# Optimization experiments

Hardware: AMD Instinct MI355X
Metric: run time of the kernel (lower is better)

## Reference

```python
import jax, jax.numpy as jnp
import numpy as np

K = 4          # neighbor_num
BN_EPS = 1e-5


def setup_inputs() -> dict:
    key = jax.random.key(0)
    ks = jax.random.split(key, 5)
    b, n, c = 16384, 12, 512
    x = jax.random.normal(ks[0], (b, n, c), dtype=jnp.float32)
    std = np.sqrt(2.0 / c).astype(np.float32)
    Uw = jax.random.normal(ks[1], (c, c), dtype=jnp.float32) * std
    Vw = jax.random.normal(ks[2], (c, c), dtype=jnp.float32) * std
    bound = 1.0 / np.sqrt(c)
    Ub = jax.random.uniform(ks[3], (c,), minval=-bound, maxval=bound, dtype=jnp.float32)
    Vb = jax.random.uniform(ks[4], (c,), minval=-bound, maxval=bound, dtype=jnp.float32)
    gamma = jnp.ones((n,), dtype=jnp.float32)
    beta = jnp.zeros((n,), dtype=jnp.float32)
    return {"x": x, "Uw": Uw, "Ub": Ub, "Vw": Vw, "Vb": Vb, "gamma": gamma, "beta": beta}


def reference(x, Uw, Ub, Vw, Vb, gamma, beta):
    # x: [b, n, c] with n = num_classes nodes
    # ---- dynamic top-k adjacency ('dots' metric), built on detached x ----
    si = jax.lax.stop_gradient(x)
    sim = jnp.einsum('bic,bjc->bij', si, si)                 # [b, n, n]
    thr = jax.lax.top_k(sim, K)[0][..., -1:]                 # k-th largest per row
    adj = (sim >= thr).astype(x.dtype)                       # [b, n, n]
    # ---- normalize_digraph: D^{-1/2} A D^{-1/2} (row degrees) ----
    deg_inv_sqrt = adj.sum(axis=-1) ** -0.5                  # [b, n]
    A = deg_inv_sqrt[:, :, None] * adj * deg_inv_sqrt[:, None, :]
    # ---- aggregate + projections ----
    Vx = jnp.einsum('bnc,dc->bnd', x, Vw) + Vb               # V(x)
    agg = jnp.einsum('bij,bjc->bic', A, Vx)
    h = agg + jnp.einsum('bnc,dc->bnd', x, Uw) + Ub          # aggregate + U(x)
    # ---- BatchNorm1d over node channel n (stats over batch and feature dims) ----
    mean = h.mean(axis=(0, 2))                               # [n]
    var = ((h - mean[None, :, None]) ** 2).mean(axis=(0, 2)) # biased var, [n]
    hn = (h - mean[None, :, None]) * jax.lax.rsqrt(var + BN_EPS)[None, :, None]
    hn = hn * gamma[None, :, None] + beta[None, :, None]
    return jax.nn.relu(x + hn)
```

## Files before the change

### kernel.cpp

```cpp
#include <hip/hip_runtime.h>
#include <hip/hip_fp16.h>


typedef _Float16 half8 __attribute__((ext_vector_type(8)));
typedef _Float16 half4 __attribute__((ext_vector_type(4)));
typedef float floatx4 __attribute__((ext_vector_type(4)));

#define NN 12
#define CH 512
#define NB 16384
#define M_ROWS (NB * NN)

__device__ __forceinline__ float relu_f(float v) { return v > 0.f ? v : 0.f; }

__device__ __forceinline__ void gload16(const void* g, void* l) {
    __builtin_amdgcn_global_load_lds(
        (__attribute__((address_space(1))) const unsigned int*)g,
        (__attribute__((address_space(3))) unsigned int*)l, 16, 0, 0);
}

__global__ __launch_bounds__(256) void kw_build(const float* __restrict__ Uw,
                                                const float* __restrict__ Vw,
                                                _Float16* __restrict__ Wcat,
                                                double* __restrict__ gAcc) {
    int e = blockIdx.x * 256 + threadIdx.x;
    int d = e >> 10, k = e & 1023;
    float v = (k < 512) ? Uw[d * 512 + k] : Vw[d * 512 + (k - 512)];
    Wcat[e] = (_Float16)v;
    if (blockIdx.x == 0 && threadIdx.x < 24) gAcc[threadIdx.x] = 0.0;
}

__global__ __launch_bounds__(256) void k1_adj(const float* __restrict__ x,
                                              _Float16* __restrict__ Abuf,
                                              float* __restrict__ rs,
                                              int pathA) {
    __shared__ float xs[NN][CH + 4];
    __shared__ double sim[NN][NN];
    __shared__ double thr[NN];
    __shared__ float Amat[NN][NN];
    __shared__ float dinv[NN];

    const int b = blockIdx.x, t = threadIdx.x;
    const float* xb = x + (size_t)b * NN * CH;

    for (int e = t; e < NN * CH / 4; e += 256) {
        int r = e >> 7, c4 = (e & 127) << 2;
        float4 v = ((const float4*)xb)[e];
        *(float4*)&xs[r][c4] = v;
    }
    __syncthreads();

    if (t < 78) {
        int i = 0, rem = t;
        while (rem >= NN - i) { rem -= NN - i; i++; }
        const int j = i + rem;
        double a0 = 0.0, a1 = 0.0, a2 = 0.0, a3 = 0.0;
        for (int c = 0; c < CH; c += 4) {
            float4 va = *(const float4*)&xs[i][c];
            float4 vb = *(const float4*)&xs[j][c];
            a0 += (double)va.x * (double)vb.x;
            a1 += (double)va.y * (double)vb.y;
            a2 += (double)va.z * (double)vb.z;
            a3 += (double)va.w * (double)vb.w;
        }
        double acc = (a0 + a1) + (a2 + a3);
        sim[i][j] = acc;
        sim[j][i] = acc;
    }
    __syncthreads();

    if (t < 12) {
        double a = -1e300, b2 = -1e300, c2 = -1e300, d2 = -1e300;
        for (int j = 0; j < 12; j++) {
            double v = sim[t][j];
            if (v > a)       { d2 = c2; c2 = b2; b2 = a; a = v; }
            else if (v > b2) { d2 = c2; c2 = b2; b2 = v; }
            else if (v > c2) { d2 = c2; c2 = v; }
            else if (v > d2) { d2 = v; }
        }
        thr[t] = d2;
        int deg = 0;
        for (int j = 0; j < 12; j++) deg += (sim[t][j] >= d2);
        dinv[t] = 1.0f / sqrtf((float)deg);
    }
    __syncthreads();

    if (t < 144) {
        int i = t / 12, j = t % 12;
        Amat[i][j] = (sim[i][j] >= thr[i]) ? dinv[i] * dinv[j] : 0.0f;
    }
    __syncthreads();

    if (t < 12) {
        float s = 0.f;
        for (int j = 0; j < 12; j++) s += Amat[t][j];
        rs[b * NN + t] = s;
    }

    const size_t strideK = pathA ? 1024 : 512;
    const size_t yoff = pathA ? 512 : 0;
    for (int e = t; e < NN * CH / 4; e += 256) {
        int i = e >> 7, c4 = (e & 127) << 2;
        float ax = 0.f, ay = 0.f, az = 0.f, aw = 0.f;
#pragma unroll
        for (int j = 0; j < 12; j++) {
            const float a = Amat[i][j];
            float4 v = *(const float4*)&xs[j][c4];
            ax += a * v.x; ay += a * v.y; az += a * v.z; aw += a * v.w;
        }
        const size_t row = (size_t)b * NN + i;
        half4 hy;
        hy[0] = (_Float16)ax; hy[1] = (_Float16)ay;
        hy[2] = (_Float16)az; hy[3] = (_Float16)aw;
        *(half4*)(Abuf + row * strideK + yoff + c4) = hy;
        if (pathA) {
            float4 xv = *(const float4*)&xs[i][c4];
            half4 hx;
            hx[0] = (_Float16)xv.x; hx[1] = (_Float16)xv.y;
            hx[2] = (_Float16)xv.z; hx[3] = (_Float16)xv.w;
            *(half4*)(Abuf + row * 1024 + c4) = hx;
        }
    }
}

__global__ __launch_bounds__(256) void k2_gemm(
    const _Float16* __restrict__ Abuf, const float* __restrict__ xf,
    const _Float16* __restrict__ Wcat, const float* __restrict__ rs,
    const float* __restrict__ Ub, const float* __restrict__ Vb,
    float* __restrict__ hout, double* __restrict__ gS1,
    double* __restrict__ gS2, int pathA) {
    __shared__ __align__(16) _Float16 As[128 * 32];
    __shared__ __align__(16) _Float16 Bs[128 * 32];
    __shared__ float bs1[12], bs2[12];

    const int t = threadIdx.x;
    const int bid = blockIdx.x;
    const int xcd = bid & 7, jj = bid >> 3;
    const int nt = jj & 3, mt = (jj >> 2) * 8 + xcd;
    const int m0 = mt * 128, n0 = nt * 128;
    const int lane = t & 63, wv = t >> 6;
    const int l15 = lane & 15, quad = lane >> 4;
    const int mwb = (wv & 1) * 64, nwb = (wv >> 1) * 64;
    const int srow = t >> 2, scol = (t & 3) * 8;

    _Float16* ldsA = As + wv * 512;
    _Float16* ldsB = Bs + wv * 512;

    floatx4 acc[4][4];
#pragma unroll
    for (int mi = 0; mi < 4; mi++)
#pragma unroll
        for (int ni = 0; ni < 4; ni++)
#pragma unroll
            for (int e = 0; e < 4; e++) acc[mi][ni][e] = 0.f;

    for (int kt = 0; kt < 32; kt++) {
        const int k0 = kt * 32;
        __syncthreads();
        if (pathA) {
#pragma unroll
            for (int pass = 0; pass < 2; pass++) {
                const int row = srow + pass * 64;
                const size_t grow = (size_t)(m0 + row);
                gload16(Abuf + grow * 1024 + k0 + scol, ldsA + pass * 2048);
                gload16(Wcat + (size_t)(n0 + row) * 1024 + k0 + scol,
                        ldsB + pass * 2048);
            }
        } else {
#pragma unroll
            for (int pass = 0; pass < 2; pass++) {
                const int row = srow + pass * 64;
                const size_t grow = (size_t)(m0 + row);
                if (k0 < 512) {
                    const float* p = xf + grow * 512 + k0 + scol;
                    float4 f0 = *(const float4*)p;
                    float4 f1 = *(const float4*)(p + 4);
                    half8 va;
                    va[0] = (_Float16)f0.x; va[1] = (_Float16)f0.y;
                    va[2] = (_Float16)f0.z; va[3] = (_Float16)f0.w;
                    va[4] = (_Float16)f1.x; va[5] = (_Float16)f1.y;
                    va[6] = (_Float16)f1.z; va[7] = (_Float16)f1.w;
                    *(half8*)&As[row * 32 + scol] = va;
                } else {
                    gload16(Abuf + grow * 512 + (k0 - 512) + scol,
                            ldsA + pass * 2048);
                }
                gload16(Wcat + (size_t)(n0 + row) * 1024 + k0 + scol,
                        ldsB + pass * 2048);
            }
        }
        __syncthreads();

        half8 af[4], bfr[4];
#pragma unroll
        for (int mi = 0; mi < 4; mi++)
            af[mi] = *(half8*)&As[(mwb + mi * 16 + l15) * 32 + quad * 8];
#pragma unroll
        for (int ni = 0; ni < 4; ni++)
            bfr[ni] = *(half8*)&Bs[(nwb + ni * 16 + l15) * 32 + quad * 8];
#pragma unroll
        for (int mi = 0; mi < 4; mi++)
#pragma unroll
            for (int ni = 0; ni < 4; ni++)
                acc[mi][ni] = __builtin_amdgcn_mfma_f32_16x16x32_f16(
                    af[mi], bfr[ni], acc[mi][ni], 0, 0, 0);
    }

    if (t < 12) { bs1[t] = 0.f; bs2[t] = 0.f; }
    __syncthreads();
#pragma unroll
    for (int mi = 0; mi < 4; mi++) {
#pragma unroll
        for (int r = 0; r < 4; r++) {
            const int m = m0 + mwb + mi * 16 + quad * 4 + r;
            const float rsm = rs[m];
            float p1 = 0.f, p2 = 0.f;
#pragma unroll
            for (int ni = 0; ni < 4; ni++) {
                const int d = n0 + nwb + ni * 16 + l15;
                float h = acc[mi][ni][r] + rsm * Vb[d] + Ub[d];
                hout[(size_t)m * 512 + d] = h;
                p1 += h; p2 += h * h;
            }
            for (int off = 1; off < 16; off <<= 1) {
                p1 += __shfl_xor(p1, off, 16);
                p2 += __shfl_xor(p2, off, 16);
            }
            if (l15 == 0) {
                atomicAdd(&bs1[m % 12], p1);
                atomicAdd(&bs2[m % 12], p2);
            }
        }
    }
    __syncthreads();
    if (t < 12) {
        atomicAdd(&gS1[t], (double)bs1[t]);
        atomicAdd(&gS2[t], (double)bs2[t]);
    }
}

__global__ void k3_stats(const double* __restrict__ gS1,
                         const double* __restrict__ gS2,
                         const float* __restrict__ gamma,
                         const float* __restrict__ beta,
                         float* __restrict__ bnp) {
    int t = threadIdx.x;
    if (t < 12) {
        const double cnt = (double)NB * 512.0;
        double mean = gS1[t] / cnt;
        double var = gS2[t] / cnt - mean * mean;
        float inv = rsqrtf((float)var + 1e-5f);
        float scale = gamma[t] * inv;
        bnp[t] = scale;
        bnp[12 + t] = beta[t] - (float)mean * scale;
    }
}

__global__ __launch_bounds__(256) void k4_final(const float* __restrict__ x,
                                                float* __restrict__ out,
                                                const float* __restrict__ bnp) {
    __shared__ float sc[12], sh[12];
    if (threadIdx.x < 12) {
        sc[threadIdx.x] = bnp[threadIdx.x];
        sh[threadIdx.x] = bnp[12 + threadIdx.x];
    }
    __syncthreads();
    const size_t n4 = (size_t)M_ROWS * 128;
    for (size_t i = (size_t)blockIdx.x * 256 + threadIdx.x; i < n4;
         i += (size_t)gridDim.x * 256) {
        int m = (int)(i >> 7);
        int n = m % 12;
        float4 h = ((const float4*)out)[i];
        float4 xv = ((const float4*)x)[i];
        float s = sc[n], b = sh[n];
        float4 r;
        r.x = relu_f(xv.x + h.x * s + b);
        r.y = relu_f(xv.y + h.y * s + b);
        r.z = relu_f(xv.z + h.z * s + b);
        r.w = relu_f(xv.w + h.w * s + b);
        ((float4*)out)[i] = r;
    }
}

extern "C" void kernel_launch(void* const* d_in, const int* in_sizes, int n_in,
                              void* d_out, int out_size, void* d_ws,
                              size_t ws_size, hipStream_t stream) {
    const float* x     = (const float*)d_in[0];
    const float* Uw    = (const float*)d_in[1];
    const float* Ub    = (const float*)d_in[2];
    const float* Vw    = (const float*)d_in[3];
    const float* Vb    = (const float*)d_in[4];
    const float* gamma = (const float*)d_in[5];
    const float* beta  = (const float*)d_in[6];
    float* out = (float*)d_out;

    const size_t szA  = (size_t)M_ROWS * 1024 * 2;
    const size_t szB  = (size_t)M_ROWS * 512 * 2;
    const size_t szW  = (size_t)512 * 1024 * 2;
    const size_t szrs = (size_t)M_ROWS * 4;
    const size_t needA = szA + szW + szrs + 24 * 8 + 24 * 4;
    const int pathA = (ws_size >= needA) ? 1 : 0;

    char* w = (char*)d_ws;
    _Float16* Abuf = (_Float16*)w;
    const size_t big = pathA ? szA : szB;
    _Float16* Wcat = (_Float16*)(w + big);
    float* rs      = (float*)(w + big + szW);
    double* gS1    = (double*)(w + big + szW + szrs);
    double* gS2    = gS1 + 12;
    float* bnp     = (float*)(gS2 + 12);

    kw_build<<<2048, 256, 0, stream>>>(Uw, Vw, Wcat, gS1);
    k1_adj<<<NB, 256, 0, stream>>>(x, Abuf, rs, pathA);
    k2_gemm<<<(M_ROWS / 128) * 4, 256, 0, stream>>>(Abuf, x, Wcat, rs, Ub, Vb,
                                                    out, gS1, gS2, pathA);
    k3_stats<<<1, 64, 0, stream>>>(gS1, gS2, gamma, beta, bnp);
    k4_final<<<4096, 256, 0, stream>>>(x, out, bnp);
}
```

Before: 1.413 ms.

## Double-buffer GEMM LDS with swizzle, split sim dot products, store h in fp16

The GEMM kernel now double-buffers its LDS tiles and issues the next tile's loads before computing the current one, leaving one barrier per k-step. Staging and fragment reads use an XOR column swizzle to reduce LDS bank conflicts. The adjacency kernel splits each pairwise dot product across three threads, so 234 threads work instead of 78. When workspace allows, the intermediate h is written and read back as fp16 instead of fp32, halving that traffic at some cost in precision.

```diff
diff --git a/kernel.cpp b/kernel.cpp
--- a/kernel.cpp
+++ b/kernel.cpp
@@ -35,6 +35,7 @@
                                               float* __restrict__ rs,
                                               int pathA) {
     __shared__ float xs[NN][CH + 4];
+    __shared__ double psum[78][3];
     __shared__ double sim[NN][NN];
     __shared__ double thr[NN];
     __shared__ float Amat[NN][NN];
@@ -50,12 +51,15 @@
     }
     __syncthreads();
 
-    if (t < 78) {
-        int i = 0, rem = t;
+    if (t < 234) {
+        const int p = t / 3, s = t - p * 3;
+        int i = 0, rem = p;
         while (rem >= NN - i) { rem -= NN - i; i++; }
         const int j = i + rem;
+        const int c0 = (s == 0) ? 0 : (s == 1 ? 176 : 352);
+        const int c1 = (s == 0) ? 176 : (s == 1 ? 352 : 512);
         double a0 = 0.0, a1 = 0.0, a2 = 0.0, a3 = 0.0;
-        for (int c = 0; c < CH; c += 4) {
+        for (int c = c0; c < c1; c += 4) {
             float4 va = *(const float4*)&xs[i][c];
             float4 vb = *(const float4*)&xs[j][c];
             a0 += (double)va.x * (double)vb.x;
@@ -63,7 +67,15 @@
             a2 += (double)va.z * (double)vb.z;
             a3 += (double)va.w * (double)vb.w;
         }
-        double acc = (a0 + a1) + (a2 + a3);
+        psum[p][s] = (a0 + a1) + (a2 + a3);
+    }
+    __syncthreads();
+
+    if (t < 78) {
+        int i = 0, rem = t;
+        while (rem >= NN - i) { rem -= NN - i; i++; }
+        const int j = i + rem;
+        double acc = (psum[t][0] + psum[t][1]) + psum[t][2];
         sim[i][j] = acc;
         sim[j][i] = acc;
     }
@@ -127,10 +139,10 @@
     const _Float16* __restrict__ Abuf, const float* __restrict__ xf,
     const _Float16* __restrict__ Wcat, const float* __restrict__ rs,
     const float* __restrict__ Ub, const float* __restrict__ Vb,
-    float* __restrict__ hout, double* __restrict__ gS1,
-    double* __restrict__ gS2, int pathA) {
-    __shared__ __align__(16) _Float16 As[128 * 32];
-    __shared__ __align__(16) _Float16 Bs[128 * 32];
+    float* __restrict__ hout, _Float16* __restrict__ hout16,
+    double* __restrict__ gS1, double* __restrict__ gS2, int pathA, int hpath) {
+    __shared__ __align__(16) _Float16 As[2][128 * 32];
+    __shared__ __align__(16) _Float16 Bs[2][128 * 32];
     __shared__ float bs1[12], bs2[12];
 
     const int t = threadIdx.x;
@@ -141,10 +153,9 @@
     const int lane = t & 63, wv = t >> 6;
     const int l15 = lane & 15, quad = lane >> 4;
     const int mwb = (wv & 1) * 64, nwb = (wv >> 1) * 64;
-    const int srow = t >> 2, scol = (t & 3) * 8;
-
-    _Float16* ldsA = As + wv * 512;
-    _Float16* ldsB = Bs + wv * 512;
+    const int srow = t >> 2, qs = t & 3;
+    const int fsw = (srow >> 1) & 3;
+    const int scol = (qs ^ fsw) * 8;
 
     floatx4 acc[4][4];
 #pragma unroll
@@ -154,56 +165,58 @@
 #pragma unroll
             for (int e = 0; e < 4; e++) acc[mi][ni][e] = 0.f;
 
+    auto stage = [&](int buf, int kt) {
+        const int k0 = kt * 32;
+#pragma unroll
+        for (int pass = 0; pass < 2; pass++) {
+            const int row = srow + pass * 64;
+            const size_t grow = (size_t)(m0 + row);
+            _Float16* la = &As[buf][pass * 2048 + wv * 512];
+            _Float16* lb = &Bs[buf][pass * 2048 + wv * 512];
+            if (pathA) {
+                gload16(Abuf + grow * 1024 + k0 + scol, la);
+            } else if (k0 < 512) {
+                const float* p = xf + grow * 512 + k0 + scol;
+                float4 f0 = *(const float4*)p;
+                float4 f1 = *(const float4*)(p + 4);
+                half8 va;
+                va[0] = (_Float16)f0.x; va[1] = (_Float16)f0.y;
+                va[2] = (_Float16)f0.z; va[3] = (_Float16)f0.w;
+                va[4] = (_Float16)f1.x; va[5] = (_Float16)f1.y;
+                va[6] = (_Float16)f1.z; va[7] = (_Float16)f1.w;
+                *(half8*)&As[buf][row * 32 + qs * 8] = va;
+            } else {
+                gload16(Abuf + grow * 512 + (k0 - 512) + scol, la);
+            }
+            gload16(Wcat + (size_t)(n0 + row) * 1024 + k0 + scol, lb);
+        }
+    };
+
+    stage(0, 0);
+    __syncthreads();
+
+    const int rcol = (quad ^ ((l15 >> 1) & 3)) * 8;
+
+    int cur = 0;
     for (int kt = 0; kt < 32; kt++) {
-        const int k0 = kt * 32;
-        __syncthreads();
-        if (pathA) {
-#pragma unroll
-            for (int pass = 0; pass < 2; pass++) {
-                const int row = srow + pass * 64;
-                const size_t grow = (size_t)(m0 + row);
-                gload16(Abuf + grow * 1024 + k0 + scol, ldsA + pass * 2048);
-                gload16(Wcat + (size_t)(n0 + row) * 1024 + k0 + scol,
-                        ldsB + pass * 2048);
-            }
-        } else {
-#pragma unroll
-            for (int pass = 0; pass < 2; pass++) {
-                const int row = srow + pass * 64;
-                const size_t grow = (size_t)(m0 + row);
-                if (k0 < 512) {
-                    const float* p = xf + grow * 512 + k0 + scol;
-                    float4 f0 = *(const float4*)p;
-                    float4 f1 = *(const float4*)(p + 4);
-                    half8 va;
-                    va[0] = (_Float16)f0.x; va[1] = (_Float16)f0.y;
-                    va[2] = (_Float16)f0.z; va[3] = (_Float16)f0.w;
-                    va[4] = (_Float16)f1.x; va[5] = (_Float16)f1.y;
-                    va[6] = (_Float16)f1.z; va[7] = (_Float16)f1.w;
-                    *(half8*)&As[row * 32 + scol] = va;
-                } else {
-                    gload16(Abuf + grow * 512 + (k0 - 512) + scol,
-                            ldsA + pass * 2048);
-                }
-                gload16(Wcat + (size_t)(n0 + row) * 1024 + k0 + scol,
-                        ldsB + pass * 2048);
-            }
-        }
-        __syncthreads();
+        if (kt < 31) stage(cur ^ 1, kt + 1);
 
         half8 af[4], bfr[4];
 #pragma unroll
         for (int mi = 0; mi < 4; mi++)
-            af[mi] = *(half8*)&As[(mwb + mi * 16 + l15) * 32 + quad * 8];
+            af[mi] = *(half8*)&As[cur][(mwb + mi * 16 + l15) * 32 + rcol];
 #pragma unroll
         for (int ni = 0; ni < 4; ni++)
-            bfr[ni] = *(half8*)&Bs[(nwb + ni * 16 + l15) * 32 + quad * 8];
+            bfr[ni] = *(half8*)&Bs[cur][(nwb + ni * 16 + l15) * 32 + rcol];
 #pragma unroll
         for (int mi = 0; mi < 4; mi++)
 #pragma unroll
             for (int ni = 0; ni < 4; ni++)
                 acc[mi][ni] = __builtin_amdgcn_mfma_f32_16x16x32_f16(
                     af[mi], bfr[ni], acc[mi][ni], 0, 0, 0);
+
+        __syncthreads();
+        cur ^= 1;
     }
 
     if (t < 12) { bs1[t] = 0.f; bs2[t] = 0.f; }
@@ -219,7 +232,8 @@
             for (int ni = 0; ni < 4; ni++) {
                 const int d = n0 + nwb + ni * 16 + l15;
                 float h = acc[mi][ni][r] + rsm * Vb[d] + Ub[d];
-                hout[(size_t)m * 512 + d] = h;
+                if (hpath) hout16[(size_t)m * 512 + d] = (_Float16)h;
+                else       hout[(size_t)m * 512 + d] = h;
                 p1 += h; p2 += h * h;
             }
             for (int off = 1; off < 16; off <<= 1) {
@@ -258,7 +272,9 @@
 
 __global__ __launch_bounds__(256) void k4_final(const float* __restrict__ x,
                                                 float* __restrict__ out,
-                                                const float* __restrict__ bnp) {
+                                                const _Float16* __restrict__ h16,
+                                                const float* __restrict__ bnp,
+                                                int hpath) {
     __shared__ float sc[12], sh[12];
     if (threadIdx.x < 12) {
         sc[threadIdx.x] = bnp[threadIdx.x];
@@ -270,7 +286,14 @@
          i += (size_t)gridDim.x * 256) {
         int m = (int)(i >> 7);
         int n = m % 12;
-        float4 h = ((const float4*)out)[i];
+        float4 h;
+        if (hpath) {
+            half4 hv = *(const half4*)(h16 + i * 4);
+            h.x = (float)hv[0]; h.y = (float)hv[1];
+            h.z = (float)hv[2]; h.w = (float)hv[3];
+        } else {
+            h = ((const float4*)out)[i];
+        }
         float4 xv = ((const float4*)x)[i];
         float s = sc[n], b = sh[n];
         float4 r;
@@ -298,8 +321,10 @@
     const size_t szB  = (size_t)M_ROWS * 512 * 2;
     const size_t szW  = (size_t)512 * 1024 * 2;
     const size_t szrs = (size_t)M_ROWS * 4;
+    const size_t szH  = (size_t)M_ROWS * 512 * 2;
     const size_t needA = szA + szW + szrs + 24 * 8 + 24 * 4;
     const int pathA = (ws_size >= needA) ? 1 : 0;
+    const int hpath = (pathA && ws_size >= needA + szH) ? 1 : 0;
 
     char* w = (char*)d_ws;
     _Float16* Abuf = (_Float16*)w;
@@ -309,11 +334,13 @@
     double* gS1    = (double*)(w + big + szW + szrs);
     double* gS2    = gS1 + 12;
     float* bnp     = (float*)(gS2 + 12);
+    _Float16* Hbuf = (_Float16*)(w + needA);
 
     kw_build<<<2048, 256, 0, stream>>>(Uw, Vw, Wcat, gS1);
     k1_adj<<<NB, 256, 0, stream>>>(x, Abuf, rs, pathA);
     k2_gemm<<<(M_ROWS / 128) * 4, 256, 0, stream>>>(Abuf, x, Wcat, rs, Ub, Vb,
-                                                    out, gS1, gS2, pathA);
+                                                    out, Hbuf, gS1, gS2, pathA,
+                                                    hpath);
     k3_stats<<<1, 64, 0, stream>>>(gS1, gS2, gamma, beta, bnp);
-    k4_final<<<4096, 256, 0, stream>>>(x, out, bnp);
-}
+    k4_final<<<4096, 256, 0, stream>>>(x, out, Hbuf, bnp, hpath);
+}
```

New measurement: 1.235 ms. 12.6% less time.
